# Kernel optimization log

Hardware: AMD Instinct MI355X
Metric: run time of the kernel (lower is better)

The kernel has to match this reference:

```python
import jax, jax.numpy as jnp
import numpy as np

B, N, T, IN_DIM, OUT_DIM = 16, 500, 12, 2, 2
H, D, K, NH, NBLOCKS, T_OUT, GDEP = 64, 64, 10, 24, 2, 12, 2
H2 = 2 * H


def setup_inputs():
    key = jax.random.key(0)
    ks = iter(jax.random.split(key, 64))

    def rn(shape, s=1.0):
        return jax.random.normal(next(ks), shape, dtype=jnp.float32) * s

    def z(*shape):
        return jnp.zeros(shape, jnp.float32)

    sI = 1.0 / np.sqrt(IN_DIM)
    sH = 1.0 / np.sqrt(H)
    sH2 = 1.0 / np.sqrt(H2)
    sD = 1.0 / np.sqrt(D)
    adj = jax.random.uniform(next(ks), (N, N), dtype=jnp.float32)
    inp = {
        'x': rn((B, N, T, IN_DIM)),
        'weather': rn((B, T, 4)),
        'geo_adj': adj / adj.sum(1, keepdims=True),
        'fcx_W': rn((IN_DIM, H), sI), 'fcx_b': z(H),
        'env_cb': rn((K, D)), 'nodes_cb': rn((N, D)),
        'w_v': rn((D, K), sD), 'w_k': rn((D, D), sD), 'w_q': rn((D, D), sD),
        'core_W': rn((H, H * H), sH), 'core_b': z(H * H),
        'tcnN_Win': rn((K, H2, H2), sH2), 'tcnN_bin': z(K, H2),
        'tcnN_Wf': rn((K, NBLOCKS, 2, H2, H2), sH2), 'tcnN_bf': z(K, NBLOCKS, H2),
        'tcnN_Wg': rn((K, NBLOCKS, 2, H2, H2), sH2), 'tcnN_bg': z(K, NBLOCKS, H2),
        'tcnN_Wout': rn((K, H2, H), sH2), 'tcnN_bout': z(K, H),
        'tcnP_Win': rn((K, H2, H2), sH2), 'tcnP_bin': z(K, H2),
        'tcnP_Wf': rn((K, NBLOCKS, 2, H2, H2), sH2), 'tcnP_bf': z(K, NBLOCKS, H2),
        'tcnP_Wg': rn((K, NBLOCKS, 2, H2, H2), sH2), 'tcnP_bg': z(K, NBLOCKS, H2),
        'tcnP_Wout': rn((K, H2, H), sH2), 'tcnP_bout': z(K, H),
        'bn1_g': jnp.ones((H,), jnp.float32), 'bn1_b': z(H),
        'bnP_g': jnp.ones((H,), jnp.float32), 'bnP_b': z(H),
        'gcn1_W': rn((H, H), sH), 'gcn1_b': z(H),
        'gcn2_W': rn((H, H), sH), 'gcn2_b': z(H),
        'gcnp_W': rn((H, H), sH), 'gcnp_b': z(H),
        'nv_p1': rn((2 * NH, H)), 'nv_p2': rn((N, H)), 'nv_p3': rn((N, H)),
        'nv_pk': rn((H, H, H), sH),
        'out_W1': rn((T_OUT, H, 100), sH), 'out_b1': z(T_OUT, 100),
        'out_W2': rn((T_OUT, 100, OUT_DIM), 0.1), 'out_b2': z(T_OUT, OUT_DIM),
        't_pos': jax.random.randint(next(ks), (B, T, 2), 0, 7),
        'ind': jax.random.randint(next(ks), (B, T, 2), 0, 7),
    }
    return inp


def _tstep_emb(t, dim):
    half = dim // 2
    freqs = jnp.exp(-jnp.log(10000.0) * jnp.arange(half, dtype=jnp.float32) / half)
    a = t.astype(jnp.float32)[:, None] * freqs[None]
    return jnp.concatenate([jnp.cos(a), jnp.sin(a)], -1)


def _conv2(h, W, b, d):
    # causal kernel-2 dilated conv over time: h [B,N,T,C], W [2,C,Co] -> [B,N,T-d,Co]
    return (jnp.einsum('bntc,co->bnto', h[:, :, :-d], W[0])
            + jnp.einsum('bntc,co->bnto', h[:, :, d:], W[1]) + b)


def _tcn(xin, Win, bin_, Wf, bf, Wg, bg, Wout, bout):
    # gated dilated TCN (Graph-WaveNet style), per node over time
    h = jnp.einsum('bntc,co->bnto', xin, Win) + bin_
    for l in range(Wf.shape[0]):
        d = 2 ** l
        f = jnp.tanh(_conv2(h, Wf[l], bf[l], d))
        g = jax.nn.sigmoid(_conv2(h, Wg[l], bg[l], d))
        h = f * g + h[:, :, d:, :]
    return jnp.einsum('bntc,ch->bnth', h, Wout) + bout


def _bn(h, g, b):
    # BatchNorm1d over channels, stats over (batch, nodes); training mode
    mu = h.mean((0, 1))
    var = h.var((0, 1))
    return g * (h - mu) * jax.lax.rsqrt(var + 1e-5) + b


def _gcn(h, adj, W, b):
    # multi-hop diffusion: sum_{k=0..GDEP} A^k h, then linear
    eq = 'nm,bmh->bnh' if adj.ndim == 2 else 'bnm,bmh->bnh'
    acc, zt = h, h
    for _ in range(GDEP):
        zt = jnp.einsum(eq, adj, zt)
        acc = acc + zt
    return jnp.einsum('bnh,ho->bno', acc, W) + b


def _forward(x, weather, geo_adj, fcx_W, fcx_b, env_cb, nodes_cb, w_v, w_k, w_q,
             core_W, core_b,
             tcnN_Win, tcnN_bin, tcnN_Wf, tcnN_bf, tcnN_Wg, tcnN_bg, tcnN_Wout, tcnN_bout,
             tcnP_Win, tcnP_bin, tcnP_Wf, tcnP_bf, tcnP_Wg, tcnP_bg, tcnP_Wout, tcnP_bout,
             bn1_g, bn1_b, bnP_g, bnP_b, gcn1_W, gcn1_b, gcn2_W, gcn2_b, gcnp_W, gcnp_b,
             nv_p1, nv_p2, nv_p3, nv_pk, out_W1, out_b1, out_W2, out_b2, t_pos, ind):
    scale = 1.0 / jnp.sqrt(jnp.float32(D))
    ind_p = jnp.where(ind[:, :, 0] <= 4, ind[:, :, 1], NH - 1 + ind[:, :, 1])
    tp = jnp.where(t_pos[:, :, 0] <= 4, t_pos[:, :, 1], NH - 1 + t_pos[:, :, 1])
    t_emb = _tstep_emb(tp.reshape(-1), H).reshape(B, T, H)

    # codebook attention -> hard cluster assignment (gumbel softmax, straight-through)
    mat_v = env_cb @ w_v
    mat_k = env_cb @ w_k
    mat_q = nodes_cb @ w_q
    scores = jax.nn.softmax((mat_q @ mat_k.T) * scale, axis=1)
    logits = scores @ mat_v                                   # [N,K]
    gn = jax.random.gumbel(jax.random.key(42), logits.shape, dtype=logits.dtype)
    y_soft = jax.nn.softmax(logits + gn, axis=1)
    hard = jax.nn.one_hot(jnp.argmax(y_soft, axis=1), K, dtype=y_soft.dtype)
    mask = y_soft + jax.lax.stop_gradient(hard - y_soft)      # [N,K] one-hot fwd

    x_emb = jnp.einsum('bnti,ih->bnth', x, fcx_W) + fcx_b
    total_x = jnp.concatenate(
        [x_emb, jnp.broadcast_to(t_emb[:, None], (B, N, T, H))], -1)  # [B,N,T,2H]

    unbias = jnp.zeros((B, N, H), total_x.dtype)
    h_prev = jnp.zeros((B, N, H), total_x.dtype)
    for i in range(K):  # small fixed cluster count
        m = mask[:, i]
        xm = total_x * m[None, :, None, None]
        hn = _tcn(xm[:, :, 1:], tcnN_Win[i], tcnN_bin[i], tcnN_Wf[i], tcnN_bf[i],
                  tcnN_Wg[i], tcnN_bg[i], tcnN_Wout[i], tcnN_bout[i])[:, :, 0, :]
        hp = _tcn(xm[:, :, :-1], tcnP_Win[i], tcnP_bin[i], tcnP_Wf[i], tcnP_bf[i],
                  tcnP_Wg[i], tcnP_bg[i], tcnP_Wout[i], tcnP_bout[i])[:, :, 0, :]
        unbias = unbias + m[None, :, None] * hn
        h_prev = h_prev + m[None, :, None] * hp

    unbias = _bn(unbias, bn1_g, bn1_b)
    h_prev = _bn(h_prev, bnP_g, bnP_b)

    h1 = _gcn(h_prev, geo_adj, gcn1_W, gcn1_b)
    core = (t_emb[:, T - 1] @ core_W + core_b).reshape(B, H, H)
    causal = jax.nn.softmax(jnp.einsum('bnh,bhk,bmk->bnm', unbias, core, h_prev), axis=-1)
    h2 = _gcn(unbias, causal, gcn2_W, gcn2_b)

    te = nv_p1[ind_p[:, -(T - 1)]]                            # [B,H]
    adp = jnp.einsum('ai,ijk->ajk', te, nv_pk)
    adp = jnp.einsum('bj,ajk->abk', nv_p2, adp)
    adp = jnp.einsum('ck,abk->abc', nv_p3, adp)
    adp = jax.nn.softmax(jax.nn.relu(adp), axis=2)            # [B,N,N]
    h3 = _gcn(unbias, adp, gcnp_W, gcnp_b)

    cur_h = h1 + h2 + h3
    hmid = jax.nn.elu(jnp.einsum('bnh,thf->bntf', cur_h, out_W1) + out_b1)
    return jnp.einsum('bntf,tfo->bnto', hmid, out_W2) + out_b2  # [B,N,T_OUT,OUT_DIM]


def reference(x, weather, geo_adj, fcx_W, fcx_b, env_cb, nodes_cb, w_v, w_k, w_q,
              core_W, core_b,
              tcnN_Win, tcnN_bin, tcnN_Wf, tcnN_bf, tcnN_Wg, tcnN_bg, tcnN_Wout, tcnN_bout,
              tcnP_Win, tcnP_bin, tcnP_Wf, tcnP_bf, tcnP_Wg, tcnP_bg, tcnP_Wout, tcnP_bout,
              bn1_g, bn1_b, bnP_g, bnP_b, gcn1_W, gcn1_b, gcn2_W, gcn2_b, gcnp_W, gcnp_b,
              nv_p1, nv_p2, nv_p3, nv_pk, out_W1, out_b1, out_W2, out_b2, t_pos, ind):
    return _forward(x, weather, geo_adj, fcx_W, fcx_b, env_cb, nodes_cb, w_v, w_k, w_q,
                    core_W, core_b,
                    tcnN_Win, tcnN_bin, tcnN_Wf, tcnN_bf, tcnN_Wg, tcnN_bg, tcnN_Wout, tcnN_bout,
                    tcnP_Win, tcnP_bin, tcnP_Wf, tcnP_bf, tcnP_Wg, tcnP_bg, tcnP_Wout, tcnP_bout,
                    bn1_g, bn1_b, bnP_g, bnP_b, gcn1_W, gcn1_b, gcn2_W, gcn2_b, gcnp_W, gcnp_b,
                    nv_p1, nv_p2, nv_p3, nv_pk, out_W1, out_b1, out_W2, out_b2, t_pos, ind)
```

## Files before the change

kernel.cpp:

```cpp
#include <hip/hip_runtime.h>
#include <hip/hip_bf16.h>
#include <math.h>

#define B_ 16
#define N_ 500
#define T_ 12
#define K_ 10
#define NROWS (B_*N_)
#define TROWS 6
#define NTCN2 2688

__device__ __forceinline__ unsigned rotl32(unsigned v, int r){ return (v<<r)|(v>>(32-r)); }

__device__ __forceinline__ void threefry2x32(unsigned k0, unsigned k1,
                                             unsigned c0, unsigned c1,
                                             unsigned &o0, unsigned &o1){
  unsigned ks2 = k0 ^ k1 ^ 0x1BD11BDAu;
  unsigned x0 = c0 + k0, x1 = c1 + k1;
#define TF_R(r) { x0 += x1; x1 = rotl32(x1,(r)); x1 ^= x0; }
  TF_R(13) TF_R(15) TF_R(26) TF_R(6)
  x0 += k1;  x1 += ks2 + 1u;
  TF_R(17) TF_R(29) TF_R(16) TF_R(24)
  x0 += ks2; x1 += k0 + 2u;
  TF_R(13) TF_R(15) TF_R(26) TF_R(6)
// ... 508 lines not shown
  }
  __syncthreads();

  {
    int o6 = tid & 63, grp = tid >> 6;
    #pragma unroll
    for (int ii=0; ii<2; ++ii){
      int i = grp*2 + ii;
      if (i >= TROWS) continue;
      float acc = 0.f;
      for (int c = 0; c < 128; c += 4){
        float w0=Wout[(c+0)*64+o6], w1=Wout[(c+1)*64+o6],
              w2=Wout[(c+2)*64+o6], w3=Wout[(c+3)*64+o6];
        float4 xv = *(const float4*)&sH2[i*128 + c];
        acc += xv.x*w0 + xv.y*w1 + xv.z*w2 + xv.w*w3;
      }
      if (rowBN[i] >= 0) outb[rowBN[i]*64 + o6] = acc + bout[o6];
    }
  }
}

__global__ __launch_bounds__(256) void k_bnstats(const float* __restrict__ unb,
                                                 const float* __restrict__ hpr,
                                                 float* __restrict__ stats){
  int bid = blockIdx.x;
  int tensor = bid >> 6, c = bid & 63;
  const float* buf = tensor ? hpr : unb;
  float s1 = 0.f, s2 = 0.f;
  for (int r = threadIdx.x; r < NROWS; r += 256){
    float v = buf[r*64 + c];
    s1 += v; s2 += v*v;
  }
  __shared__ float r1[256], r2[256];
  r1[threadIdx.x]=s1; r2[threadIdx.x]=s2;
  __syncthreads();
  for (int s=128; s>0; s>>=1){
    if (threadIdx.x < s){ r1[threadIdx.x]+=r1[threadIdx.x+s]; r2[threadIdx.x]+=r2[threadIdx.x+s]; }
    __syncthreads();
  }
  if (threadIdx.x==0){
    float mean = r1[0]/(float)NROWS;
    float var  = r2[0]/(float)NROWS - mean*mean;
    stats[tensor*128 + c]      = mean;
    stats[tensor*128 + 64 + c] = rsqrtf(var + 1e-5f);
  }
}

__global__ __launch_bounds__(256) void k_bnapply(float* __restrict__ unb, float* __restrict__ hpr,
                                                 const float* __restrict__ stats,
                                                 const float* __restrict__ g1, const float* __restrict__ be1,
                                                 const float* __restrict__ gP, const float* __restrict__ beP){
  int idx = blockIdx.x*256 + threadIdx.x;
  if (idx >= 2*NROWS*64) return;
  int tensor = idx >= NROWS*64;
  int local = idx - tensor*NROWS*64;
  int c = local & 63;
  float* buf = tensor ? hpr : unb;
  float mean = stats[tensor*128+c], rstd = stats[tensor*128+64+c];
  float g = tensor ? gP[c] : g1[c];
  float bb = tensor ? beP[c] : be1[c];
  buf[local] = g * (buf[local]-mean) * rstd + bb;
}

template<int AMODE, int RELU, int FINAL, int ADD>
__global__ __launch_bounds__(256) void k_attn(
    const float* __restrict__ geo,
    const float* __restrict__ Qf, const float* __restrict__ Qb,
    const float* __restrict__ M,
    const float* __restrict__ Keysf, const float* __restrict__ Keysb,
    const float* __restrict__ X,
    const float* __restrict__ X0, const float* __restrict__ Z1,
    const float* __restrict__ Wg, const float* __restrict__ bg,
    float* __restrict__ cur, float* __restrict__ Y)
{
  __shared__ __align__(16) float kbuf[64][65];
  __shared__ __align__(16) float xbuf[64][64];
  __shared__ __align__(16) float vbuf[16][64];
  __shared__ __align__(16) float pbuf[16][64];

  int b = blockIdx.y, n0 = blockIdx.x*16;
  int tid = threadIdx.x;
  int nl = tid >> 5, ml = tid & 31;
  int nA = n0 + nl, nB = n0 + nl + 8;
  float rrK[16], rrX[16], rrA[4];

  if (AMODE != 0){
    for (int idx = tid; idx < 1024; idx += 256){
      int r = idx >> 6, kk = idx & 63;
      int nn = n0 + r;
      float q = 0.f;
      if (nn < N_) q = (AMODE == 1) ? Qf[(b*N_+nn)*64+kk] : Qb[nn*64+kk];
      pbuf[r][kk] = q;
    }
    for (int idx = tid; idx < 4096; idx += 256)
      kbuf[idx>>6][idx&63] = M[b*4096 + idx];
    __syncthreads();
    float vxA = 0.f, vyA = 0.f, vxB = 0.f, vyB = 0.f;
    for (int kk = 0; kk < 64; ++kk){
      float qA = pbuf[nl][kk], qB = pbuf[nl+8][kk];
      float2 m2 = *(const float2*)&kbuf[kk][ml*2];
      vxA += qA*m2.x; vyA += qA*m2.y;
      vxB += qB*m2.x; vyB += qB*m2.y;
    }
    __syncthreads();
    vbuf[nl  ][ml*2] = vxA; vbuf[nl  ][ml*2+1] = vyA;
    vbuf[nl+8][ml*2] = vxB; vbuf[nl+8][ml*2+1] = vyB;
  }
  {
    if (AMODE != 0) __syncthreads();
    #pragma unroll
    for (int ii = 0; ii < 16; ++ii){
      int idx = tid + ii*256;
      int mm = idx >> 6, kk = idx & 63;
      if (AMODE != 0)
        kbuf[mm][kk] = (AMODE == 1) ? Keysf[(b*N_+mm)*64+kk] : Keysb[mm*64+kk];
      xbuf[mm][kk] = X[(b*N_+mm)*64+kk];
    }
    if (AMODE == 0){
      #pragma unroll
      for (int ii = 0; ii < 4; ++ii){
        int idx = tid + ii*256;
        int r = idx >> 6, mm = idx & 63;
        int nn = n0 + r;
        pbuf[r][mm] = (nn < N_) ? geo[nn*N_ + mm] : 0.f;
      }
    }
    __syncthreads();
  }

  float m_runA = -1e30f, l_runA = 0.f;
  float m_runB = -1e30f, l_runB = 0.f;
  float accxA = 0.f, accyA = 0.f, accxB = 0.f, accyB = 0.f;

  for (int ci = 0; ci < 8; ++ci){
    int m0 = ci*64;
    if (ci < 7){
      #pragma unroll
      for (int ii=0; ii<16; ++ii){
        int idx = tid + ii*256;
        int mm = idx >> 6, kk = idx & 63;
        int m = m0 + 64 + mm;
        if (AMODE != 0)
          rrK[ii] = (m < N_) ? ((AMODE == 1) ? Keysf[(b*N_+m)*64+kk] : Keysb[m*64+kk]) : 0.f;
        rrX[ii] = (m < N_) ? X[(b*N_+m)*64+kk] : 0.f;
      }
      if (AMODE == 0){
        #pragma unroll
        for (int ii=0; ii<4; ++ii){
          int idx = tid + ii*256;
          int r = idx >> 6, mm = idx & 63;
          int nn = n0 + r, m = m0 + 64 + mm;
          rrA[ii] = (nn < N_ && m < N_) ? geo[nn*N_ + m] : 0.f;
        }
      }
    }
    if (AMODE != 0){
      float s0A = 0.f, s1A = 0.f, s0B = 0.f, s1B = 0.f;
      for (int kk = 0; kk < 64; kk += 4){
        float4 qA = *(const float4*)&vbuf[nl  ][kk];
        float4 qB = *(const float4*)&vbuf[nl+8][kk];
        float4 k0 = *(const float4*)&kbuf[ml   ][kk];
        float4 k1 = *(const float4*)&kbuf[ml+32][kk];
        s0A += qA.x*k0.x + qA.y*k0.y + qA.z*k0.z + qA.w*k0.w;
        s1A += qA.x*k1.x + qA.y*k1.y + qA.z*k1.z + qA.w*k1.w;
        s0B += qB.x*k0.x + qB.y*k0.y + qB.z*k0.z + qB.w*k0.w;
        s1B += qB.x*k1.x + qB.y*k1.y + qB.z*k1.z + qB.w*k1.w;
      }
      float v0A = (m0 + ml      < N_) ? (RELU ? fmaxf(s0A, 0.f) : s0A) : -1e30f;
      float v1A = (m0 + ml + 32 < N_) ? (RELU ? fmaxf(s1A, 0.f) : s1A) : -1e30f;
      float v0B = (m0 + ml      < N_) ? (RELU ? fmaxf(s0B, 0.f) : s0B) : -1e30f;
      float v1B = (m0 + ml + 32 < N_) ? (RELU ? fmaxf(s1B, 0.f) : s1B) : -1e30f;
      float cmaxA = fmaxf(v0A, v1A), cmaxB = fmaxf(v0B, v1B);
      #pragma unroll
      for (int msk = 1; msk < 32; msk <<= 1){
        cmaxA = fmaxf(cmaxA, __shfl_xor(cmaxA, msk, 32));
        cmaxB = fmaxf(cmaxB, __shfl_xor(cmaxB, msk, 32));
      }
      float mnewA = fmaxf(m_runA, cmaxA), mnewB = fmaxf(m_runB, cmaxB);
      float scaleA = expf(m_runA - mnewA), scaleB = expf(m_runB - mnewB);
      float p0A = expf(v0A - mnewA), p1A = expf(v1A - mnewA);
      float p0B = expf(v0B - mnewB), p1B = expf(v1B - mnewB);
      float lcA = p0A + p1A, lcB = p0B + p1B;
      #pragma unroll
      for (int msk = 1; msk < 32; msk <<= 1){
        lcA += __shfl_xor(lcA, msk, 32);
        lcB += __shfl_xor(lcB, msk, 32);
      }
      l_runA = l_runA*scaleA + lcA; m_runA = mnewA;
      l_runB = l_runB*scaleB + lcB; m_runB = mnewB;
      accxA *= scaleA; accyA *= scaleA;
      accxB *= scaleB; accyB *= scaleB;
      pbuf[nl  ][ml]    = p0A;
      pbuf[nl  ][ml+32] = p1A;
      pbuf[nl+8][ml]    = p0B;
      pbuf[nl+8][ml+32] = p1B;
    }
    __syncthreads();
    for (int mm = 0; mm < 64; mm += 4){
      float4 pA = *(const float4*)&pbuf[nl  ][mm];
      float4 pB = *(const float4*)&pbuf[nl+8][mm];
      float2 x0 = *(const float2*)&xbuf[mm+0][ml*2];
      float2 x1 = *(const float2*)&xbuf[mm+1][ml*2];
      float2 x2 = *(const float2*)&xbuf[mm+2][ml*2];
      float2 x3 = *(const float2*)&xbuf[mm+3][ml*2];
      accxA += pA.x*x0.x + pA.y*x1.x + pA.z*x2.x + pA.w*x3.x;
      accyA += pA.x*x0.y + pA.y*x1.y + pA.z*x2.y + pA.w*x3.y;
      accxB += pB.x*x0.x + pB.y*x1.x + pB.z*x2.x + pB.w*x3.x;
      accyB += pB.x*x0.y + pB.y*x1.y + pB.z*x2.y + pB.w*x3.y;
    }
    __syncthreads();
    if (ci < 7){
      #pragma unroll
      for (int ii=0; ii<16; ++ii){
        int idx = tid + ii*256;
        int mm = idx >> 6, kk = idx & 63;
        if (AMODE != 0) kbuf[mm][kk] = rrK[ii];
        xbuf[mm][kk] = rrX[ii];
      }
      if (AMODE == 0){
        #pragma unroll
        for (int ii=0; ii<4; ++ii){
          int idx = tid + ii*256;
          pbuf[idx>>6][idx&63] = rrA[ii];
        }
      }
      __syncthreads();
    }
  }
  if (AMODE != 0){
    float invA = 1.f / l_runA, invB = 1.f / l_runB;
    accxA *= invA; accyA *= invA;
    accxB *= invB; accyB *= invB;
  }

  if (!FINAL){
    if (nA < N_){
      float2 o2; o2.x = accxA; o2.y = accyA;
      *(float2*)&Y[(b*N_+nA)*64 + ml*2] = o2;
    }
    if (nB < N_){
      float2 o2; o2.x = accxB; o2.y = accyB;
      *(float2*)&Y[(b*N_+nB)*64 + ml*2] = o2;
    }
    return;
  }

  {
    float svxA = 0.f, svyA = 0.f, svxB = 0.f, svyB = 0.f;
    if (nA < N_){
      int row = b*N_ + nA;
      float2 x0v = *(const float2*)&X0[row*64 + ml*2];
      float2 z1v = *(const float2*)&Z1[row*64 + ml*2];
      svxA = accxA + x0v.x + z1v.x;
      svyA = accyA + x0v.y + z1v.y;
    }
    if (nB < N_){
      int row = b*N_ + nB;
      float2 x0v = *(const float2*)&X0[row*64 + ml*2];
      float2 z1v = *(const float2*)&Z1[row*64 + ml*2];
      svxB = accxB + x0v.x + z1v.x;
      svyB = accyB + x0v.y + z1v.y;
    }
    vbuf[nl  ][ml*2] = svxA; vbuf[nl  ][ml*2+1] = svyA;
    vbuf[nl+8][ml*2] = svxB; vbuf[nl+8][ml*2+1] = svyB;
    for (int idx = tid; idx < 4096; idx += 256)
      kbuf[idx>>6][idx&63] = Wg[idx];
    __syncthreads();
    float oxA = 0.f, oyA = 0.f, oxB = 0.f, oyB = 0.f;
    for (int kk = 0; kk < 64; ++kk){
      float sA = vbuf[nl][kk], sB = vbuf[nl+8][kk];
      float2 w2 = *(const float2*)&kbuf[kk][ml*2];
      oxA += sA*w2.x; oyA += sA*w2.y;
      oxB += sB*w2.x; oyB += sB*w2.y;
    }
    float2 bv = *(const float2*)&bg[ml*2];
    if (nA < N_){
      int row = b*N_ + nA;
      float vx = oxA + bv.x, vy = oyA + bv.y;
      if (ADD){
        float2 old = *(const float2*)&cur[row*64 + ml*2];
        vx += old.x; vy += old.y;
      }
      float2 o2; o2.x = vx; o2.y = vy;
      *(float2*)&cur[row*64 + ml*2] = o2;
    }
    if (nB < N_){
      int row = b*N_ + nB;
      float vx = oxB + bv.x, vy = oyB + bv.y;
      if (ADD){
        float2 old = *(const float2*)&cur[row*64 + ml*2];
        vx += old.x; vy += old.y;
      }
      float2 o2; o2.x = vx; o2.y = vy;
      *(float2*)&cur[row*64 + ml*2] = o2;
    }
  }
}

template<int AMODE, int RELU>
__global__ __launch_bounds__(256) void k_attn_p1(
    const float* __restrict__ Qf, const float* __restrict__ Qb,
    const float* __restrict__ M,
    const float* __restrict__ Keysf, const float* __restrict__ Keysb,
    const float* __restrict__ X,
    float* __restrict__ Pb, float* __restrict__ Y)
{
  __shared__ __align__(16) float kbuf[64][65];
  __shared__ __align__(16) float xbuf[64][64];
  __shared__ __align__(16) float vbuf[16][64];
  __shared__ __align__(16) float pbuf[16][64];

  int b = blockIdx.y, n0 = blockIdx.x*16;
  int tid = threadIdx.x;
  int nl = tid >> 5, ml = tid & 31;
  int nA = n0 + nl, nB = n0 + nl + 8;
  float rrK[16], rrX[16];

  for (int idx = tid; idx < 1024; idx += 256){
    int r = idx >> 6, kk = idx & 63;
    int nn = n0 + r;
    float q = 0.f;
    if (nn < N_) q = (AMODE == 1) ? Qf[(b*N_+nn)*64+kk] : Qb[nn*64+kk];
    pbuf[r][kk] = q;
  }
  for (int idx = tid; idx < 4096; idx += 256)
    kbuf[idx>>6][idx&63] = M[b*4096 + idx];
  __syncthreads();
  float vxA = 0.f, vyA = 0.f, vxB = 0.f, vyB = 0.f;
  for (int kk = 0; kk < 64; ++kk){
    float qA = pbuf[nl][kk], qB = pbuf[nl+8][kk];
    float2 m2 = *(const float2*)&kbuf[kk][ml*2];
    vxA += qA*m2.x; vyA += qA*m2.y;
    vxB += qB*m2.x; vyB += qB*m2.y;
  }
  __syncthreads();
  vbuf[nl  ][ml*2] = vxA; vbuf[nl  ][ml*2+1] = vyA;
  vbuf[nl+8][ml*2] = vxB; vbuf[nl+8][ml*2+1] = vyB;
  __syncthreads();
  #pragma unroll
  for (int ii = 0; ii < 16; ++ii){
    int idx = tid + ii*256;
    int mm = idx >> 6, kk = idx & 63;
    kbuf[mm][kk] = (AMODE == 1) ? Keysf[(b*N_+mm)*64+kk] : Keysb[mm*64+kk];
    xbuf[mm][kk] = X[(b*N_+mm)*64+kk];
  }
  __syncthreads();

  float m_runA = -1e30f, l_runA = 0.f;
  float m_runB = -1e30f, l_runB = 0.f;
  float accxA = 0.f, accyA = 0.f, accxB = 0.f, accyB = 0.f;

  for (int ci = 0; ci < 8; ++ci){
    int m0 = ci*64;
    if (ci < 7){
      #pragma unroll
      for (int ii=0; ii<16; ++ii){
        int idx = tid + ii*256;
        int mm = idx >> 6, kk = idx & 63;
        int m = m0 + 64 + mm;
        rrK[ii] = (m < N_) ? ((AMODE == 1) ? Keysf[(b*N_+m)*64+kk] : Keysb[m*64+kk]) : 0.f;
        rrX[ii] = (m < N_) ? X[(b*N_+m)*64+kk] : 0.f;
      }
    }
    {
      float s0A = 0.f, s1A = 0.f, s0B = 0.f, s1B = 0.f;
      for (int kk = 0; kk < 64; kk += 4){
        float4 qA = *(const float4*)&vbuf[nl  ][kk];
        float4 qB = *(const float4*)&vbuf[nl+8][kk];
        float4 k0 = *(const float4*)&kbuf[ml   ][kk];
        float4 k1 = *(const float4*)&kbuf[ml+32][kk];
        s0A += qA.x*k0.x + qA.y*k0.y + qA.z*k0.z + qA.w*k0.w;
        s1A += qA.x*k1.x + qA.y*k1.y + qA.z*k1.z + qA.w*k1.w;
        s0B += qB.x*k0.x + qB.y*k0.y + qB.z*k0.z + qB.w*k0.w;
        s1B += qB.x*k1.x + qB.y*k1.y + qB.z*k1.z + qB.w*k1.w;
      }
      float v0A = (m0 + ml      < N_) ? (RELU ? fmaxf(s0A, 0.f) : s0A) : -1e30f;
      float v1A = (m0 + ml + 32 < N_) ? (RELU ? fmaxf(s1A, 0.f) : s1A) : -1e30f;
      float v0B = (m0 + ml      < N_) ? (RELU ? fmaxf(s0B, 0.f) : s0B) : -1e30f;
      float v1B = (m0 + ml + 32 < N_) ? (RELU ? fmaxf(s1B, 0.f) : s1B) : -1e30f;
      if (nA < N_){
        Pb[((long)(b*N_+nA))*512 + m0 + ml]      = v0A;
        Pb[((long)(b*N_+nA))*512 + m0 + ml + 32] = v1A;
      }
      if (nB < N_){
        Pb[((long)(b*N_+nB))*512 + m0 + ml]      = v0B;
        Pb[((long)(b*N_+nB))*512 + m0 + ml + 32] = v1B;
      }
      float cmaxA = fmaxf(v0A, v1A), cmaxB = fmaxf(v0B, v1B);
      #pragma unroll
      for (int msk = 1; msk < 32; msk <<= 1){
        cmaxA = fmaxf(cmaxA, __shfl_xor(cmaxA, msk, 32));
        cmaxB = fmaxf(cmaxB, __shfl_xor(cmaxB, msk, 32));
      }
      float mnewA = fmaxf(m_runA, cmaxA), mnewB = fmaxf(m_runB, cmaxB);
      float scaleA = expf(m_runA - mnewA), scaleB = expf(m_runB - mnewB);
      float p0A = expf(v0A - mnewA), p1A = expf(v1A - mnewA);
      float p0B = expf(v0B - mnewB), p1B = expf(v1B - mnewB);
      float lcA = p0A + p1A, lcB = p0B + p1B;
      #pragma unroll
      for (int msk = 1; msk < 32; msk <<= 1){
        lcA += __shfl_xor(lcA, msk, 32);
        lcB += __shfl_xor(lcB, msk, 32);
      }
      l_runA = l_runA*scaleA + lcA; m_runA = mnewA;
      l_runB = l_runB*scaleB + lcB; m_runB = mnewB;
      accxA *= scaleA; accyA *= scaleA;
      accxB *= scaleB; accyB *= scaleB;
      pbuf[nl  ][ml]    = p0A;
      pbuf[nl  ][ml+32] = p1A;
      pbuf[nl+8][ml]    = p0B;
      pbuf[nl+8][ml+32] = p1B;
    }
    __syncthreads();
    for (int mm = 0; mm < 64; mm += 4){
      float4 pA = *(const float4*)&pbuf[nl  ][mm];
      float4 pB = *(const float4*)&pbuf[nl+8][mm];
      float2 x0 = *(const float2*)&xbuf[mm+0][ml*2];
      float2 x1 = *(const float2*)&xbuf[mm+1][ml*2];
      float2 x2 = *(const float2*)&xbuf[mm+2][ml*2];
      float2 x3 = *(const float2*)&xbuf[mm+3][ml*2];
      accxA += pA.x*x0.x + pA.y*x1.x + pA.z*x2.x + pA.w*x3.x;
      accyA += pA.x*x0.y + pA.y*x1.y + pA.z*x2.y + pA.w*x3.y;
      accxB += pB.x*x0.x + pB.y*x1.x + pB.z*x2.x + pB.w*x3.x;
      accyB += pB.x*x0.y + pB.y*x1.y + pB.z*x2.y + pB.w*x3.y;
    }
    __syncthreads();
    if (ci < 7){
      #pragma unroll
      for (int ii=0; ii<16; ++ii){
        int idx = tid + ii*256;
        kbuf[idx>>6][idx&63] = rrK[ii];
        xbuf[idx>>6][idx&63] = rrX[ii];
      }
      __syncthreads();
    }
  }
  float invA = 1.f / l_runA, invB = 1.f / l_runB;
  accxA *= invA; accyA *= invA;
  accxB *= invB; accyB *= invB;
  if (nA < N_){
    float2 o2; o2.x = accxA; o2.y = accyA;
    *(float2*)&Y[(b*N_+nA)*64 + ml*2] = o2;
  }
  if (nB < N_){
    float2 o2; o2.x = accxB; o2.y = accyB;
    *(float2*)&Y[(b*N_+nB)*64 + ml*2] = o2;
  }
}

template<int ADD>
__global__ __launch_bounds__(256) void k_attn_p2(
    const float* __restrict__ Pb,
    const float* __restrict__ X,
    const float* __restrict__ X0,
    const float* __restrict__ Wg, const float* __restrict__ bg,
    float* __restrict__ cur)
{
  __shared__ __align__(16) float pbuf[16][516];
  __shared__ __align__(16) float xbuf[64][64];
  __shared__ __align__(16) float vbuf[16][64];

  int b = blockIdx.y, n0 = blockIdx.x*16;
  int tid = threadIdx.x;
  int nl = tid >> 5, ml = tid & 31;
  int nA = n0 + nl, nB = n0 + nl + 8;
  float rrX[16];

  for (int idx = tid; idx < 16*512; idx += 256){
    int r = idx >> 9, m = idx & 511;
    int nn = n0 + r;
    pbuf[r][m] = (nn < N_) ? Pb[((long)(b*N_+nn))*512 + m] : -1e30f;
  }
  __syncthreads();
  float lmaxA = -1e30f, lmaxB = -1e30f;
  for (int m = ml; m < 512; m += 32){
    lmaxA = fmaxf(lmaxA, pbuf[nl  ][m]);
    lmaxB = fmaxf(lmaxB, pbuf[nl+8][m]);
  }
  #pragma unroll
  for (int msk=1; msk<32; msk<<=1){
    lmaxA = fmaxf(lmaxA, __shfl_xor(lmaxA, msk, 32));
    lmaxB = fmaxf(lmaxB, __shfl_xor(lmaxB, msk, 32));
  }
  float lsumA = 0.f, lsumB = 0.f;
  for (int m = ml; m < 512; m += 32){
    float pA = expf(pbuf[nl  ][m] - lmaxA);
    float pB = expf(pbuf[nl+8][m] - lmaxB);
    pbuf[nl  ][m] = pA;
    pbuf[nl+8][m] = pB;
    lsumA += pA; lsumB += pB;
  }
  #pragma unroll
  for (int msk=1; msk<32; msk<<=1){
    lsumA += __shfl_xor(lsumA, msk, 32);
    lsumB += __shfl_xor(lsumB, msk, 32);
  }
  float invA = 1.f/lsumA, invB = 1.f/lsumB;
  for (int m = ml; m < 512; m += 32){
    pbuf[nl  ][m] *= invA;
    pbuf[nl+8][m] *= invB;
  }

  #pragma unroll
  for (int ii=0; ii<16; ++ii){
    int idx = tid + ii*256;
    int mm = idx>>6, kk = idx&63;
    xbuf[mm][kk] = X[(b*N_+mm)*64+kk];
  }
  __syncthreads();

  float accxA = 0.f, accyA = 0.f, accxB = 0.f, accyB = 0.f;
  for (int ci = 0; ci < 8; ++ci){
    int m0 = ci*64;
    if (ci < 7){
      #pragma unroll
      for (int ii=0; ii<16; ++ii){
        int idx = tid + ii*256;
        int mm = idx>>6, kk = idx&63;
        int m = m0+64+mm;
        rrX[ii] = (m < N_) ? X[(b*N_+m)*64+kk] : 0.f;
      }
    }
    for (int mm = 0; mm < 64; mm += 4){
      float4 pA = *(const float4*)&pbuf[nl  ][m0+mm];
      float4 pB = *(const float4*)&pbuf[nl+8][m0+mm];
      float2 x0 = *(const float2*)&xbuf[mm+0][ml*2];
      float2 x1 = *(const float2*)&xbuf[mm+1][ml*2];
      float2 x2 = *(const float2*)&xbuf[mm+2][ml*2];
      float2 x3 = *(const float2*)&xbuf[mm+3][ml*2];
      accxA += pA.x*x0.x + pA.y*x1.x + pA.z*x2.x + pA.w*x3.x;
      accyA += pA.x*x0.y + pA.y*x1.y + pA.z*x2.y + pA.w*x3.y;
      accxB += pB.x*x0.x + pB.y*x1.x + pB.z*x2.x + pB.w*x3.x;
      accyB += pB.x*x0.y + pB.y*x1.y + pB.z*x2.y + pB.w*x3.y;
    }
    __syncthreads();
    if (ci < 7){
      #pragma unroll
      for (int ii=0; ii<16; ++ii){
        int idx = tid + ii*256;
        xbuf[idx>>6][idx&63] = rrX[ii];
      }
      __syncthreads();
    }
  }

  {
    float svxA = 0.f, svyA = 0.f, svxB = 0.f, svyB = 0.f;
    if (nA < N_){
      int row = b*N_ + nA;
      float2 x0v = *(const float2*)&X0[row*64 + ml*2];
      float2 z1v = *(const float2*)&X[row*64 + ml*2];
      svxA = accxA + x0v.x + z1v.x;
      svyA = accyA + x0v.y + z1v.y;
    }
    if (nB < N_){
      int row = b*N_ + nB;
      float2 x0v = *(const float2*)&X0[row*64 + ml*2];
      float2 z1v = *(const float2*)&X[row*64 + ml*2];
      svxB = accxB + x0v.x + z1v.x;
      svyB = accyB + x0v.y + z1v.y;
    }
    vbuf[nl  ][ml*2] = svxA; vbuf[nl  ][ml*2+1] = svyA;
    vbuf[nl+8][ml*2] = svxB; vbuf[nl+8][ml*2+1] = svyB;
    for (int idx = tid; idx < 4096; idx += 256)
      xbuf[idx>>6][idx&63] = Wg[idx];
    __syncthreads();
    float oxA = 0.f, oyA = 0.f, oxB = 0.f, oyB = 0.f;
    for (int kk = 0; kk < 64; ++kk){
      float sA = vbuf[nl][kk], sB = vbuf[nl+8][kk];
      float2 w2 = *(const float2*)&xbuf[kk][ml*2];
      oxA += sA*w2.x; oyA += sA*w2.y;
      oxB += sB*w2.x; oyB += sB*w2.y;
    }
    float2 bv = *(const float2*)&bg[ml*2];
    if (nA < N_){
      int row = b*N_ + nA;
      float vx = oxA + bv.x, vy = oyA + bv.y;
      if (ADD){
        float2 old = *(const float2*)&cur[row*64 + ml*2];
        vx += old.x; vy += old.y;
      }
      float2 o2; o2.x = vx; o2.y = vy;
      *(float2*)&cur[row*64 + ml*2] = o2;
    }
    if (nB < N_){
      int row = b*N_ + nB;
      float vx = oxB + bv.x, vy = oyB + bv.y;
      if (ADD){
        float2 old = *(const float2*)&cur[row*64 + ml*2];
        vx += old.x; vy += old.y;
      }
      float2 o2; o2.x = vx; o2.y = vy;
      *(float2*)&cur[row*64 + ml*2] = o2;
    }
  }
}

__global__ __launch_bounds__(128) void k_out(const float* __restrict__ cur,
                                             const float* __restrict__ W1, const float* __restrict__ bb1,
                                             const float* __restrict__ W2, const float* __restrict__ bb2,
                                             float* __restrict__ out){
  __shared__ float ch[4][64];
  __shared__ float hid[4*1200];
  int tid = threadIdx.x;
  int rbase = blockIdx.x*4;
  for (int idx = tid; idx < 256; idx += 128){
    int r = idx >> 6, h = idx & 63;
    ch[r][h] = cur[(rbase+r)*64 + h];
  }
  __syncthreads();
  for (int job = tid; job < 1200; job += 128){
    int t = job / 100, f = job - t*100;
    float a0 = bb1[t*100+f], a1 = a0, a2 = a0, a3 = a0;
    for (int h = 0; h < 64; ++h){
      float w = W1[(t*64+h)*100 + f];
      a0 += ch[0][h]*w; a1 += ch[1][h]*w; a2 += ch[2][h]*w; a3 += ch[3][h]*w;
    }
    hid[0*1200+job] = (a0 > 0.f) ? a0 : expm1f(a0);
    hid[1*1200+job] = (a1 > 0.f) ? a1 : expm1f(a1);
    hid[2*1200+job] = (a2 > 0.f) ? a2 : expm1f(a2);
    hid[3*1200+job] = (a3 > 0.f) ? a3 : expm1f(a3);
  }
  __syncthreads();
  if (tid < 96){
    int r = tid / 24, rem = tid % 24;
    int t = rem >> 1, o = rem & 1;
    float a = bb2[t*2+o];
    const float* hp = hid + r*1200 + t*100;
    for (int f = 0; f < 100; ++f) a += hp[f] * W2[(t*100+f)*2+o];
    out[(rbase+r)*24 + t*2+o] = a;
  }
}

extern "C" void kernel_launch(void* const* d_in, const int* in_sizes, int n_in,
                              void* d_out, int out_size, void* d_ws, size_t ws_size,
                              hipStream_t stream)
{
  const float* x        = (const float*)d_in[0];
  const float* geo      = (const float*)d_in[2];
  const float* fcx_W    = (const float*)d_in[3];
  const float* fcx_b    = (const float*)d_in[4];
  const float* env_cb   = (const float*)d_in[5];
  const float* nodes_cb = (const float*)d_in[6];
  const float* w_v      = (const float*)d_in[7];
  const float* w_k      = (const float*)d_in[8];
  const float* w_q      = (const float*)d_in[9];
  const float* core_W   = (const float*)d_in[10];
  const float* core_b   = (const float*)d_in[11];
  const float* tN_Win   = (const float*)d_in[12];
  const float* tN_bin   = (const float*)d_in[13];
  const float* tN_Wf    = (const float*)d_in[14];
  const float* tN_bf    = (const float*)d_in[15];
  const float* tN_Wg    = (const float*)d_in[16];
  const float* tN_bg    = (const float*)d_in[17];
  const float* tN_Wout  = (const float*)d_in[18];
  const float* tN_bout  = (const float*)d_in[19];
  const float* tP_Win   = (const float*)d_in[20];
  const float* tP_bin   = (const float*)d_in[21];
  const float* tP_Wf    = (const float*)d_in[22];
  const float* tP_bf    = (const float*)d_in[23];
  const float* tP_Wg    = (const float*)d_in[24];
  const float* tP_bg    = (const float*)d_in[25];
  const float* tP_Wout  = (const float*)d_in[26];
  const float* tP_bout  = (const float*)d_in[27];
  const float* bn1_g    = (const float*)d_in[28];
  const float* bn1_b    = (const float*)d_in[29];
  const float* bnP_g    = (const float*)d_in[30];
  const float* bnP_b    = (const float*)d_in[31];
  const float* gcn1_W   = (const float*)d_in[32];
  const float* gcn1_b   = (const float*)d_in[33];
  const float* gcn2_W   = (const float*)d_in[34];
  const float* gcn2_b   = (const float*)d_in[35];
  const float* gcnp_W   = (const float*)d_in[36];
  const float* gcnp_b   = (const float*)d_in[37];
  const float* nv_p1    = (const float*)d_in[38];
  const float* nv_p2    = (const float*)d_in[39];
  const float* nv_p3    = (const float*)d_in[40];
  const float* nv_pk    = (const float*)d_in[41];
  const float* out_W1   = (const float*)d_in[42];
  const float* out_b1   = (const float*)d_in[43];
  const float* out_W2   = (const float*)d_in[44];
  const float* out_b2   = (const float*)d_in[45];
  const int*   t_pos    = (const int*)d_in[46];
  const int*   ind      = (const int*)d_in[47];

  int* node_list = (int*)d_ws;
  int* off       = node_list + 512;
  float* F = (float*)((char*)d_ws + 4096);
  float* temb   = F + 0;
  float* core_f = F + 12288;
  float* tmp1   = F + 77824;
  float* stats  = F + 143360;
  float* matq   = F + 143616;
  float* unb    = F + 175616;
  float* hpr    = F + 687616;
  float* cur    = F + 1199616;
  float* zt1    = F + 1711616;
  float* Pb     = F + 2223616;
  float* TE     = Pb;
  bool useP = ws_size >= (size_t)(4096 + (size_t)(2223616 + 4096000)*4);

  k_matq <<<dim3(125), dim3(256), 0, stream>>>(nodes_cb, w_q, matq);
  k_route<<<dim3(1),   dim3(256), 0, stream>>>(env_cb, w_v, w_k, matq, node_list, off);
  k_temb <<<dim3(1),   dim3(192), 0, stream>>>(t_pos, temb);
  k_core <<<dim3(256), dim3(256), 0, stream>>>(temb, core_W, core_b, core_f);
  if (useP){
    k_tprep<<<dim3(20, 81), dim3(128), 0, stream>>>(temb, fcx_W, fcx_b, tN_Win, tP_Win, TE);
    k_tcn2 <<<dim3(NTCN2), dim3(256), 0, stream>>>(x, TE, node_list, off,
        tN_bin, tN_Wf, tN_bf, tN_Wg, tN_bg, tN_Wout, tN_bout,
        tP_bin, tP_Wf, tP_bf, tP_Wg, tP_bg, tP_Wout, tP_bout,
        unb, hpr);
  } else {
    k_tcn  <<<dim3(20, 334), dim3(256), 0, stream>>>(x, fcx_W, fcx_b, temb, node_list, off,
        tN_Win, tN_bin, tN_Wf, tN_bf, tN_Wg, tN_bg, tN_Wout, tN_bout,
        tP_Win, tP_bin, tP_Wf, tP_bf, tP_Wg, tP_bg, tP_Wout, tP_bout,
        unb, hpr);
  }
  k_bnstats<<<dim3(128), dim3(256), 0, stream>>>(unb, hpr, stats);
  k_bnapply<<<dim3(4000),dim3(256), 0, stream>>>(unb, hpr, stats, bn1_g, bn1_b, bnP_g, bnP_b);
  k_tmp1<<<dim3(256), dim3(256), 0, stream>>>(ind, nv_p1, nv_pk, tmp1);

  dim3 ag(32, 16);
  const float* nil = nullptr;
  k_attn<0,0,0,0><<<ag, 256, 0, stream>>>(geo, nil,nil,nil, nil,nil,
                                 hpr, nil,nil, nil,nil, nullptr, zt1);
  k_attn<0,0,1,0><<<ag, 256, 0, stream>>>(geo, nil,nil,nil, nil,nil,
                                 zt1, hpr, zt1, gcn1_W, gcn1_b, cur, nullptr);
  if (useP){
    k_attn_p1<1,0><<<ag, 256, 0, stream>>>(unb, nil, core_f, hpr, nil, unb, Pb, zt1);
    k_attn_p2<1>  <<<ag, 256, 0, stream>>>(Pb, zt1, unb, gcn2_W, gcn2_b, cur);
  } else {
    k_attn<1,0,0,0><<<ag, 256, 0, stream>>>(nil, unb,nil, core_f, hpr,nil,
                                   unb, nil,nil, nil,nil, nullptr, zt1);
    k_attn<1,0,1,1><<<ag, 256, 0, stream>>>(nil, unb,nil, core_f, hpr,nil,
                                   zt1, unb, zt1, gcn2_W, gcn2_b, cur, nullptr);
  }
  if (useP){
    k_attn_p1<2,1><<<ag, 256, 0, stream>>>(nil, nv_p2, tmp1, nil, nv_p3, unb, Pb, zt1);
    k_attn_p2<1>  <<<ag, 256, 0, stream>>>(Pb, zt1, unb, gcnp_W, gcnp_b, cur);
  } else {
    k_attn<2,1,0,0><<<ag, 256, 0, stream>>>(nil, nil,nv_p2, tmp1, nil,nv_p3,
                                   unb, nil,nil, nil,nil, nullptr, zt1);
    k_attn<2,1,1,1><<<ag, 256, 0, stream>>>(nil, nil,nv_p2, tmp1, nil,nv_p3,
                                   zt1, unb, zt1, gcnp_W, gcnp_b, cur, nullptr);
  }
  k_out<<<dim3(2000), dim3(128), 0, stream>>>(cur, out_W1, out_b1, out_W2, out_b2, (float*)d_out);
}
```

Baseline: 883.2 us.

## Split attention PV accumulation over key halves with float4 outputs; widen k_out rows

The P·X accumulation in three attention kernels is reorganised so each lane handles four output columns over half of the 64-key chunk. The two halves are combined with a cross-lane shuffle at the end, and outputs and epilogue loads become float4. This raises per-lane register reuse and vector width for LDS reads, at the cost of half the lanes idling in the epilogue. Separately, k_out now processes 8 rows per block instead of 4, halving the grid and reusing each W1 load across more rows.

```diff
diff --git a/kernel.cpp b/kernel.cpp
--- a/kernel.cpp
+++ b/kernel.cpp
@@ -614,6 +614,8 @@
   int tid = threadIdx.x;
   int nl = tid >> 5, ml = tid & 31;
   int nA = n0 + nl, nB = n0 + nl + 8;
+  int mh = (ml >> 4) << 5;
+  int d0 = (ml & 15) * 4;
   float rrK[16], rrX[16], rrA[4];
 
   if (AMODE != 0){
@@ -662,7 +664,8 @@
 
   float m_runA = -1e30f, l_runA = 0.f;
   float m_runB = -1e30f, l_runB = 0.f;
-  float accxA = 0.f, accyA = 0.f, accxB = 0.f, accyB = 0.f;
+  float accA[4] = {0.f,0.f,0.f,0.f};
+  float accB[4] = {0.f,0.f,0.f,0.f};
 
   for (int ci = 0; ci < 8; ++ci){
     int m0 = ci*64;
@@ -720,25 +723,30 @@
       }
       l_runA = l_runA*scaleA + lcA; m_runA = mnewA;
       l_runB = l_runB*scaleB + lcB; m_runB = mnewB;
-      accxA *= scaleA; accyA *= scaleA;
-      accxB *= scaleB; accyB *= scaleB;
+      #pragma unroll
+      for (int d=0; d<4; ++d){ accA[d] *= scaleA; accB[d] *= scaleB; }
       pbuf[nl  ][ml]    = p0A;
       pbuf[nl  ][ml+32] = p1A;
       pbuf[nl+8][ml]    = p0B;
       pbuf[nl+8][ml+32] = p1B;
     }
     __syncthreads();
-    for (int mm = 0; mm < 64; mm += 4){
-      float4 pA = *(const float4*)&pbuf[nl  ][mm];
-      float4 pB = *(const float4*)&pbuf[nl+8][mm];
-      float2 x0 = *(const float2*)&xbuf[mm+0][ml*2];
-      float2 x1 = *(const float2*)&xbuf[mm+1][ml*2];
-      float2 x2 = *(const float2*)&xbuf[mm+2][ml*2];
-      float2 x3 = *(const float2*)&xbuf[mm+3][ml*2];
-      accxA += pA.x*x0.x + pA.y*x1.x + pA.z*x2.x + pA.w*x3.x;
-      accyA += pA.x*x0.y + pA.y*x1.y + pA.z*x2.y + pA.w*x3.y;
-      accxB += pB.x*x0.x + pB.y*x1.x + pB.z*x2.x + pB.w*x3.x;
-      accyB += pB.x*x0.y + pB.y*x1.y + pB.z*x2.y + pB.w*x3.y;
+    #pragma unroll
+    for (int mm = 0; mm < 32; mm += 4){
+      float4 pA = *(const float4*)&pbuf[nl  ][mh + mm];
+      float4 pB = *(const float4*)&pbuf[nl+8][mh + mm];
+      float4 x0 = *(const float4*)&xbuf[mh+mm+0][d0];
+      float4 x1 = *(const float4*)&xbuf[mh+mm+1][d0];
+      float4 x2 = *(const float4*)&xbuf[mh+mm+2][d0];
+      float4 x3 = *(const float4*)&xbuf[mh+mm+3][d0];
+      accA[0] += pA.x*x0.x + pA.y*x1.x + pA.z*x2.x + pA.w*x3.x;
+      accA[1] += pA.x*x0.y + pA.y*x1.y + pA.z*x2.y + pA.w*x3.y;
+      accA[2] += pA.x*x0.z + pA.y*x1.z + pA.z*x2.z + pA.w*x3.z;
+      accA[3] += pA.x*x0.w + pA.y*x1.w + pA.z*x2.w + pA.w*x3.w;
+      accB[0] += pB.x*x0.x + pB.y*x1.x + pB.z*x2.x + pB.w*x3.x;
+      accB[1] += pB.x*x0.y + pB.y*x1.y + pB.z*x2.y + pB.w*x3.y;
+      accB[2] += pB.x*x0.z + pB.y*x1.z + pB.z*x2.z + pB.w*x3.z;
+      accB[3] += pB.x*x0.w + pB.y*x1.w + pB.z*x2.w + pB.w*x3.w;
     }
     __syncthreads();
     if (ci < 7){
@@ -759,42 +767,55 @@
       __syncthreads();
     }
   }
+  #pragma unroll
+  for (int d=0; d<4; ++d){
+    accA[d] += __shfl_xor(accA[d], 16, 32);
+    accB[d] += __shfl_xor(accB[d], 16, 32);
+  }
   if (AMODE != 0){
     float invA = 1.f / l_runA, invB = 1.f / l_runB;
-    accxA *= invA; accyA *= invA;
-    accxB *= invB; accyB *= invB;
+    #pragma unroll
+    for (int d=0; d<4; ++d){ accA[d] *= invA; accB[d] *= invB; }
   }
 
   if (!FINAL){
-    if (nA < N_){
-      float2 o2; o2.x = accxA; o2.y = accyA;
-      *(float2*)&Y[(b*N_+nA)*64 + ml*2] = o2;
-    }
-    if (nB < N_){
-      float2 o2; o2.x = accxB; o2.y = accyB;
-      *(float2*)&Y[(b*N_+nB)*64 + ml*2] = o2;
+    if (ml < 16){
+      if (nA < N_){
+        float4 o4; o4.x = accA[0]; o4.y = accA[1]; o4.z = accA[2]; o4.w = accA[3];
+        *(float4*)&Y[(b*N_+nA)*64 + d0] = o4;
+      }
+      if (nB < N_){
+        float4 o4; o4.x = accB[0]; o4.y = accB[1]; o4.z = accB[2]; o4.w = accB[3];
+        *(float4*)&Y[(b*N_+nB)*64 + d0] = o4;
+      }
     }
     return;
   }
 
   {
-    float svxA = 0.f, svyA = 0.f, svxB = 0.f, svyB = 0.f;
-    if (nA < N_){
-      int row = b*N_ + nA;
-      float2 x0v = *(const float2*)&X0[row*64 + ml*2];
-      float2 z1v = *(const float2*)&Z1[row*64 + ml*2];
-      svxA = accxA + x0v.x + z1v.x;
-      svyA = accyA + x0v.y + z1v.y;
-    }
-    if (nB < N_){
-      int row = b*N_ + nB;
-      float2 x0v = *(const float2*)&X0[row*64 + ml*2];
-      float2 z1v = *(const float2*)&Z1[row*64 + ml*2];
-      svxB = accxB + x0v.x + z1v.x;
-      svyB = accyB + x0v.y + z1v.y;
-    }
-    vbuf[nl  ][ml*2] = svxA; vbuf[nl  ][ml*2+1] = svyA;
-    vbuf[nl+8][ml*2] = svxB; vbuf[nl+8][ml*2+1] = svyB;
+    if (ml < 16){
+      float4 svA = {0.f,0.f,0.f,0.f}, svB = {0.f,0.f,0.f,0.f};
+      if (nA < N_){
+        int row = b*N_ + nA;
+        float4 x0v = *(const float4*)&X0[row*64 + d0];
+        float4 z1v = *(const float4*)&Z1[row*64 + d0];
+        svA.x = accA[0] + x0v.x + z1v.x;
+        svA.y = accA[1] + x0v.y + z1v.y;
+        svA.z = accA[2] + x0v.z + z1v.z;
+        svA.w = accA[3] + x0v.w + z1v.w;
+      }
+      if (nB < N_){
+        int row = b*N_ + nB;
+        float4 x0v = *(const float4*)&X0[row*64 + d0];
+        float4 z1v = *(const float4*)&Z1[row*64 + d0];
+        svB.x = accB[0] + x0v.x + z1v.x;
+        svB.y = accB[1] + x0v.y + z1v.y;
+        svB.z = accB[2] + x0v.z + z1v.z;
+        svB.w = accB[3] + x0v.w + z1v.w;
+      }
+      *(float4*)&vbuf[nl  ][d0] = svA;
+      *(float4*)&vbuf[nl+8][d0] = svB;
+    }
     for (int idx = tid; idx < 4096; idx += 256)
       kbuf[idx>>6][idx&63] = Wg[idx];
     __syncthreads();
@@ -846,6 +867,8 @@
   int tid = threadIdx.x;
   int nl = tid >> 5, ml = tid & 31;
   int nA = n0 + nl, nB = n0 + nl + 8;
+  int mh = (ml >> 4) << 5;
+  int d0 = (ml & 15) * 4;
   float rrK[16], rrX[16];
 
   for (int idx = tid; idx < 1024; idx += 256){
@@ -880,7 +903,8 @@
 
   float m_runA = -1e30f, l_runA = 0.f;
   float m_runB = -1e30f, l_runB = 0.f;
-  float accxA = 0.f, accyA = 0.f, accxB = 0.f, accyB = 0.f;
+  float accA[4] = {0.f,0.f,0.f,0.f};
+  float accB[4] = {0.f,0.f,0.f,0.f};
 
   for (int ci = 0; ci < 8; ++ci){
     int m0 = ci*64;
@@ -936,25 +960,30 @@
       }
       l_runA = l_runA*scaleA + lcA; m_runA = mnewA;
       l_runB = l_runB*scaleB + lcB; m_runB = mnewB;
-      accxA *= scaleA; accyA *= scaleA;
-      accxB *= scaleB; accyB *= scaleB;
+      #pragma unroll
+      for (int d=0; d<4; ++d){ accA[d] *= scaleA; accB[d] *= scaleB; }
       pbuf[nl  ][ml]    = p0A;
       pbuf[nl  ][ml+32] = p1A;
       pbuf[nl+8][ml]    = p0B;
       pbuf[nl+8][ml+32] = p1B;
     }
     __syncthreads();
-    for (int mm = 0; mm < 64; mm += 4){
-      float4 pA = *(const float4*)&pbuf[nl  ][mm];
-      float4 pB = *(const float4*)&pbuf[nl+8][mm];
-      float2 x0 = *(const float2*)&xbuf[mm+0][ml*2];
-      float2 x1 = *(const float2*)&xbuf[mm+1][ml*2];
-      float2 x2 = *(const float2*)&xbuf[mm+2][ml*2];
-      float2 x3 = *(const float2*)&xbuf[mm+3][ml*2];
-      accxA += pA.x*x0.x + pA.y*x1.x + pA.z*x2.x + pA.w*x3.x;
-      accyA += pA.x*x0.y + pA.y*x1.y + pA.z*x2.y + pA.w*x3.y;
-      accxB += pB.x*x0.x + pB.y*x1.x + pB.z*x2.x + pB.w*x3.x;
-      accyB += pB.x*x0.y + pB.y*x1.y + pB.z*x2.y + pB.w*x3.y;
+    #pragma unroll
+    for (int mm = 0; mm < 32; mm += 4){
+      float4 pA = *(const float4*)&pbuf[nl  ][mh + mm];
+      float4 pB = *(const float4*)&pbuf[nl+8][mh + mm];
+      float4 x0 = *(const float4*)&xbuf[mh+mm+0][d0];
+      float4 x1 = *(const float4*)&xbuf[mh+mm+1][d0];
+      float4 x2 = *(const float4*)&xbuf[mh+mm+2][d0];
+      float4 x3 = *(const float4*)&xbuf[mh+mm+3][d0];
+      accA[0] += pA.x*x0.x + pA.y*x1.x + pA.z*x2.x + pA.w*x3.x;
+      accA[1] += pA.x*x0.y + pA.y*x1.y + pA.z*x2.y + pA.w*x3.y;
+      accA[2] += pA.x*x0.z + pA.y*x1.z + pA.z*x2.z + pA.w*x3.z;
+      accA[3] += pA.x*x0.w + pA.y*x1.w + pA.z*x2.w + pA.w*x3.w;
+      accB[0] += pB.x*x0.x + pB.y*x1.x + pB.z*x2.x + pB.w*x3.x;
+      accB[1] += pB.x*x0.y + pB.y*x1.y + pB.z*x2.y + pB.w*x3.y;
+      accB[2] += pB.x*x0.z + pB.y*x1.z + pB.z*x2.z + pB.w*x3.z;
+      accB[3] += pB.x*x0.w + pB.y*x1.w + pB.z*x2.w + pB.w*x3.w;
     }
     __syncthreads();
     if (ci < 7){
@@ -967,16 +996,23 @@
       __syncthreads();
     }
   }
+  #pragma unroll
+  for (int d=0; d<4; ++d){
+    accA[d] += __shfl_xor(accA[d], 16, 32);
+    accB[d] += __shfl_xor(accB[d], 16, 32);
+  }
   float invA = 1.f / l_runA, invB = 1.f / l_runB;
-  accxA *= invA; accyA *= invA;
-  accxB *= invB; accyB *= invB;
-  if (nA < N_){
-    float2 o2; o2.x = accxA; o2.y = accyA;
-    *(float2*)&Y[(b*N_+nA)*64 + ml*2] = o2;
-  }
-  if (nB < N_){
-    float2 o2; o2.x = accxB; o2.y = accyB;
-    *(float2*)&Y[(b*N_+nB)*64 + ml*2] = o2;
+  #pragma unroll
+  for (int d=0; d<4; ++d){ accA[d] *= invA; accB[d] *= invB; }
+  if (ml < 16){
+    if (nA < N_){
+      float4 o4; o4.x = accA[0]; o4.y = accA[1]; o4.z = accA[2]; o4.w = accA[3];
+      *(float4*)&Y[(b*N_+nA)*64 + d0] = o4;
+    }
+    if (nB < N_){
+      float4 o4; o4.x = accB[0]; o4.y = accB[1]; o4.z = accB[2]; o4.w = accB[3];
+      *(float4*)&Y[(b*N_+nB)*64 + d0] = o4;
+    }
   }
 }
 
@@ -996,6 +1032,8 @@
   int tid = threadIdx.x;
   int nl = tid >> 5, ml = tid & 31;
   int nA = n0 + nl, nB = n0 + nl + 8;
+  int mh = (ml >> 4) << 5;
+  int d0 = (ml & 15) * 4;
   float rrX[16];
 
   for (int idx = tid; idx < 16*512; idx += 256){
@@ -1041,7 +1079,8 @@
   }
   __syncthreads();
 
-  float accxA = 0.f, accyA = 0.f, accxB = 0.f, accyB = 0.f;
+  float accA[4] = {0.f,0.f,0.f,0.f};
+  float accB[4] = {0.f,0.f,0.f,0.f};
   for (int ci = 0; ci < 8; ++ci){
     int m0 = ci*64;
     if (ci < 7){
@@ -1053,17 +1092,22 @@
         rrX[ii] = (m < N_) ? X[(b*N_+m)*64+kk] : 0.f;
       }
     }
-    for (int mm = 0; mm < 64; mm += 4){
-      float4 pA = *(const float4*)&pbuf[nl  ][m0+mm];
-      float4 pB = *(const float4*)&pbuf[nl+8][m0+mm];
-      float2 x0 = *(const float2*)&xbuf[mm+0][ml*2];
-      float2 x1 = *(const float2*)&xbuf[mm+1][ml*2];
-      float2 x2 = *(const float2*)&xbuf[mm+2][ml*2];
-      float2 x3 = *(const float2*)&xbuf[mm+3][ml*2];
-      accxA += pA.x*x0.x + pA.y*x1.x + pA.z*x2.x + pA.w*x3.x;
-      accyA += pA.x*x0.y + pA.y*x1.y + pA.z*x2.y + pA.w*x3.y;
-      accxB += pB.x*x0.x + pB.y*x1.x + pB.z*x2.x + pB.w*x3.x;
-      accyB += pB.x*x0.y + pB.y*x1.y + pB.z*x2.y + pB.w*x3.y;
+    #pragma unroll
+    for (int mm = 0; mm < 32; mm += 4){
+      float4 pA = *(const float4*)&pbuf[nl  ][m0 + mh + mm];
+      float4 pB = *(const float4*)&pbuf[nl+8][m0 + mh + mm];
+      float4 x0 = *(const float4*)&xbuf[mh+mm+0][d0];
+      float4 x1 = *(const float4*)&xbuf[mh+mm+1][d0];
+      float4 x2 = *(const float4*)&xbuf[mh+mm+2][d0];
+      float4 x3 = *(const float4*)&xbuf[mh+mm+3][d0];
+      accA[0] += pA.x*x0.x + pA.y*x1.x + pA.z*x2.x + pA.w*x3.x;
+      accA[1] += pA.x*x0.y + pA.y*x1.y + pA.z*x2.y + pA.w*x3.y;
+      accA[2] += pA.x*x0.z + pA.y*x1.z + pA.z*x2.z + pA.w*x3.z;
+      accA[3] += pA.x*x0.w + pA.y*x1.w + pA.z*x2.w + pA.w*x3.w;
+      accB[0] += pB.x*x0.x + pB.y*x1.x + pB.z*x2.x + pB.w*x3.x;
+      accB[1] += pB.x*x0.y + pB.y*x1.y + pB.z*x2.y + pB.w*x3.y;
+      accB[2] += pB.x*x0.z + pB.y*x1.z + pB.z*x2.z + pB.w*x3.z;
+      accB[3] += pB.x*x0.w + pB.y*x1.w + pB.z*x2.w + pB.w*x3.w;
     }
     __syncthreads();
     if (ci < 7){
@@ -1075,25 +1119,36 @@
       __syncthreads();
     }
   }
+  #pragma unroll
+  for (int d=0; d<4; ++d){
+    accA[d] += __shfl_xor(accA[d], 16, 32);
+    accB[d] += __shfl_xor(accB[d], 16, 32);
+  }
 
   {
-    float svxA = 0.f, svyA = 0.f, svxB = 0.f, svyB = 0.f;
-    if (nA < N_){
-      int row = b*N_ + nA;
-      float2 x0v = *(const float2*)&X0[row*64 + ml*2];
-      float2 z1v = *(const float2*)&X[row*64 + ml*2];
-      svxA = accxA + x0v.x + z1v.x;
-      svyA = accyA + x0v.y + z1v.y;
-    }
-    if (nB < N_){
-      int row = b*N_ + nB;
-      float2 x0v = *(const float2*)&X0[row*64 + ml*2];
-      float2 z1v = *(const float2*)&X[row*64 + ml*2];
-      svxB = accxB + x0v.x + z1v.x;
-      svyB = accyB + x0v.y + z1v.y;
-    }
-    vbuf[nl  ][ml*2] = svxA; vbuf[nl  ][ml*2+1] = svyA;
-    vbuf[nl+8][ml*2] = svxB; vbuf[nl+8][ml*2+1] = svyB;
+    if (ml < 16){
+      float4 svA = {0.f,0.f,0.f,0.f}, svB = {0.f,0.f,0.f,0.f};
+      if (nA < N_){
+        int row = b*N_ + nA;
+        float4 x0v = *(const float4*)&X0[row*64 + d0];
+        float4 z1v = *(const float4*)&X[row*64 + d0];
+        svA.x = accA[0] + x0v.x + z1v.x;
+        svA.y = accA[1] + x0v.y + z1v.y;
+        svA.z = accA[2] + x0v.z + z1v.z;
+        svA.w = accA[3] + x0v.w + z1v.w;
+      }
+      if (nB < N_){
+        int row = b*N_ + nB;
+        float4 x0v = *(const float4*)&X0[row*64 + d0];
+        float4 z1v = *(const float4*)&X[row*64 + d0];
+        svB.x = accB[0] + x0v.x + z1v.x;
+        svB.y = accB[1] + x0v.y + z1v.y;
+        svB.z = accB[2] + x0v.z + z1v.z;
+        svB.w = accB[3] + x0v.w + z1v.w;
+      }
+      *(float4*)&vbuf[nl  ][d0] = svA;
+      *(float4*)&vbuf[nl+8][d0] = svB;
+    }
     for (int idx = tid; idx < 4096; idx += 256)
       xbuf[idx>>6][idx&63] = Wg[idx];
     __syncthreads();
@@ -1132,30 +1187,36 @@
                                              const float* __restrict__ W1, const float* __restrict__ bb1,
                                              const float* __restrict__ W2, const float* __restrict__ bb2,
                                              float* __restrict__ out){
-  __shared__ float ch[4][64];
-  __shared__ float hid[4*1200];
+  __shared__ float ch[8][64];
+  __shared__ float hid[8*1200];
   int tid = threadIdx.x;
-  int rbase = blockIdx.x*4;
-  for (int idx = tid; idx < 256; idx += 128){
+  int rbase = blockIdx.x*8;
+  for (int idx = tid; idx < 512; idx += 128){
     int r = idx >> 6, h = idx & 63;
     ch[r][h] = cur[(rbase+r)*64 + h];
   }
   __syncthreads();
   for (int job = tid; job < 1200; job += 128){
     int t = job / 100, f = job - t*100;
-    float a0 = bb1[t*100+f], a1 = a0, a2 = a0, a3 = a0;
+    float bb = bb1[t*100+f];
+    float a0=bb,a1=bb,a2=bb,a3=bb,a4=bb,a5=bb,a6=bb,a7=bb;
     for (int h = 0; h < 64; ++h){
       float w = W1[(t*64+h)*100 + f];
       a0 += ch[0][h]*w; a1 += ch[1][h]*w; a2 += ch[2][h]*w; a3 += ch[3][h]*w;
+      a4 += ch[4][h]*w; a5 += ch[5][h]*w; a6 += ch[6][h]*w; a7 += ch[7][h]*w;
     }
     hid[0*1200+job] = (a0 > 0.f) ? a0 : expm1f(a0);
     hid[1*1200+job] = (a1 > 0.f) ? a1 : expm1f(a1);
     hid[2*1200+job] = (a2 > 0.f) ? a2 : expm1f(a2);
     hid[3*1200+job] = (a3 > 0.f) ? a3 : expm1f(a3);
-  }
-  __syncthreads();
-  if (tid < 96){
-    int r = tid / 24, rem = tid % 24;
+    hid[4*1200+job] = (a4 > 0.f) ? a4 : expm1f(a4);
+    hid[5*1200+job] = (a5 > 0.f) ? a5 : expm1f(a5);
+    hid[6*1200+job] = (a6 > 0.f) ? a6 : expm1f(a6);
+    hid[7*1200+job] = (a7 > 0.f) ? a7 : expm1f(a7);
+  }
+  __syncthreads();
+  for (int jb = tid; jb < 192; jb += 128){
+    int r = jb / 24, rem = jb % 24;
     int t = rem >> 1, o = rem & 1;
     float a = bb2[t*2+o];
     const float* hp = hid + r*1200 + t*100;
@@ -1276,5 +1337,5 @@
     k_attn<2,1,1,1><<<ag, 256, 0, stream>>>(nil, nil,nv_p2, tmp1, nil,nv_p3,
                                    zt1, unb, zt1, gcnp_W, gcnp_b, cur, nullptr);
   }
-  k_out<<<dim3(2000), dim3(128), 0, stream>>>(cur, out_W1, out_b1, out_W2, out_b2, (float*)d_out);
-}
+  k_out<<<dim3(1000), dim3(128), 0, stream>>>(cur, out_W1, out_b1, out_W2, out_b2, (float*)d_out);
+}
```

After: 839.5 us. 5.0% less time.
